# Optimization experiments

Hardware: AMD Instinct MI355X
Metric: run time of the kernel (lower is better)

Reference implementation:

```python
import jax, jax.numpy as jnp
import numpy as np

HIDDEN = 1024
NUM_EXPERTS = 8
TOP_K = 2
BATCH, SEQ = 4, 4096


def setup_inputs() -> dict:
    key = jax.random.key(0)
    ks = jax.random.split(key, 7)
    s = 0.02
    x = jax.random.normal(ks[0], (BATCH, SEQ, HIDDEN), dtype=jnp.float32)
    router_w = jax.random.normal(ks[1], (HIDDEN, NUM_EXPERTS), dtype=jnp.float32) * s
    router_b = jnp.zeros((NUM_EXPERTS,), dtype=jnp.float32)
    w1 = jax.random.normal(ks[2], (NUM_EXPERTS, HIDDEN, 2 * HIDDEN), dtype=jnp.float32) * s
    b1 = jnp.zeros((NUM_EXPERTS, 2 * HIDDEN), dtype=jnp.float32)
    w2 = jax.random.normal(ks[3], (NUM_EXPERTS, 2 * HIDDEN, HIDDEN), dtype=jnp.float32) * s
    b2 = jnp.zeros((NUM_EXPERTS, HIDDEN), dtype=jnp.float32)
    return {"x": x, "router_w": router_w, "router_b": router_b,
            "w1": w1, "b1": b1, "w2": w2, "b2": b2}


def reference(x, router_w, router_b, w1, b1, w2, b2):
    # Router: softmax over experts, then top-k and renormalize.
    logits = jnp.einsum("bsh,he->bse", x, router_w) + router_b        # [B,S,E]
    probs = jax.nn.softmax(logits, axis=-1)
    topk_p, topk_i = jax.lax.top_k(probs, TOP_K)                       # [B,S,K]
    topk_p = topk_p / jnp.sum(topk_p, axis=-1, keepdims=True)

    out = jnp.zeros_like(x)
    for e in range(NUM_EXPERTS):
        # combine weight for this expert (0 for tokens that didn't route here;
        # top_k indices are distinct so at most one slot matches)
        w = jnp.sum(jnp.where(topk_i == e, topk_p, 0.0), axis=-1)      # [B,S]
        h = jax.nn.relu(jnp.einsum("bsh,hf->bsf", x, w1[e]) + b1[e])   # [B,S,2H]
        y = jnp.einsum("bsf,fh->bsh", h, w2[e]) + b2[e]                # [B,S,H]
        out = out + w[..., None] * y
    return out
```

## Files before the change

### kernel.cpp

```cpp
#include <hip/hip_runtime.h>

#define HIDDEN 1024
#define FF 2048
#define NEXP 8
#define NTOK 16384
#define NPAIR (2 * NTOK)
#define MAXT 136

typedef short short8 __attribute__((ext_vector_type(8)));
typedef unsigned short ushort4v __attribute__((ext_vector_type(4)));
typedef float f32x4 __attribute__((ext_vector_type(4)));

__device__ __forceinline__ unsigned short f2b(float f) {
  union { float f; unsigned int u; } v; v.f = f;
  unsigned int u = v.u;
  return (unsigned short)((u + 0x7fffu + ((u >> 16) & 1u)) >> 16);
}
__device__ __forceinline__ float b2f(unsigned short b) {
  union { unsigned int u; float f; } v; v.u = ((unsigned int)b) << 16;
  return v.f;
}

__device__ __forceinline__ void gload16(const unsigned short* g, unsigned short* l) {
  __builtin_amdgcn_global_load_lds(
      (const __attribute__((address_space(1))) unsigned int*)g,
      (__attribute__((address_space(3))) unsigned int*)l,
      16, 0, 0);
}

#define PIPE_WAIT(n) do { \
    asm volatile("s_waitcnt vmcnt(" #n ")" ::: "memory"); \
    __builtin_amdgcn_sched_barrier(0); \
  } while (0)
#define ABAR do { \
    asm volatile("s_barrier" ::: "memory"); \
    __builtin_amdgcn_sched_barrier(0); \
  } while (0)

#define W2T_OFF 0ull
#define W1T_OFF (W2T_OFF + (unsigned long long)NEXP * HIDDEN * FF * 2)
#define XB_OFF  (W1T_OFF + (unsigned long long)NEXP * FF * HIDDEN * 2)
#define H_OFF   (XB_OFF + (unsigned long long)NTOK * HIDDEN * 2)
#define CNT_OFF (H_OFF + (unsigned long long)NPAIR * FF * 2)
#define PLIST_OFF (CNT_OFF + 256ull)
#define PW_OFF    (PLIST_OFF + (unsigned long long)NEXP * NTOK * 4)
#define TOPS_OFF  (PW_OFF + (unsigned long long)NPAIR * 4)
#define W0_OFF    (TOPS_OFF + (unsigned long long)NTOK * 4)
#define WQ_OFF    (W0_OFF + (unsigned long long)NTOK * 4)
#define YP_OFF    W1T_OFF
#define WS_NEED   (WQ_OFF + 4096ull)

__global__ void zero_out_k(float4* __restrict__ out) {
  out[(size_t)blockIdx.x * 256 + threadIdx.x] = float4{0.f, 0.f, 0.f, 0.f};
}

__global__ void transpose_cast_k(const float* __restrict__ in,
                                 unsigned short* __restrict__ out,
                                 int R, int C) {
  __shared__ float tile[32][33];
  const size_t eoff = (size_t)blockIdx.z * R * C;
  const float* inp = in + eoff;
  unsigned short* outp = out + eoff;
  const int c = threadIdx.x & 31;
  const int r0 = threadIdx.x >> 5;
  const int gr = blockIdx.y * 32, gc = blockIdx.x * 32;
#pragma unroll
  for (int i = 0; i < 4; i++) {
    int r = r0 + i * 8;
    tile[r][c] = inp[(size_t)(gr + r) * C + gc + c];
  }
  __syncthreads();
#pragma unroll
  for (int i = 0; i < 4; i++) {
    int r = r0 + i * 8;
    outp[(size_t)(gc + r) * R + gr + c] = f2b(tile[c][r]);
  }
}

__global__ void router_k(const float* __restrict__ x, const float* __restrict__ rw,
                         const float* __restrict__ rb, int* __restrict__ tops,
                         float* __restrict__ w0f, unsigned short* __restrict__ xb,
                         int* __restrict__ cnt) {
  if (blockIdx.x == 0 && threadIdx.x < NEXP) cnt[threadIdx.x] = 0;
  const int wid = threadIdx.x >> 6;
  const int lane = threadIdx.x & 63;
  const int t = blockIdx.x * 4 + wid;
  const float* xr = x + (size_t)t * HIDDEN;
  float acc[8];
#pragma unroll
  for (int e = 0; e < 8; e++) acc[e] = 0.f;
#pragma unroll
  for (int i = 0; i < 16; i++) {
    int hh = lane + 64 * i;
    float xv = xr[hh];
    const float4* rwp = reinterpret_cast<const float4*>(rw + (size_t)hh * 8);
    float4 a = rwp[0], b = rwp[1];
    acc[0] += xv * a.x; acc[1] += xv * a.y; acc[2] += xv * a.z; acc[3] += xv * a.w;
    acc[4] += xv * b.x; acc[5] += xv * b.y; acc[6] += xv * b.z; acc[7] += xv * b.w;
  }
  {
    const float4* xr4 = reinterpret_cast<const float4*>(xr);
    unsigned short* xbr = xb + (size_t)t * HIDDEN;
#pragma unroll
    for (int i = 0; i < 4; i++) {
      float4 f = xr4[lane + 64 * i];
      ushort4v o;
      o[0] = f2b(f.x); o[1] = f2b(f.y); o[2] = f2b(f.z); o[3] = f2b(f.w);
      *reinterpret_cast<ushort4v*>(&xbr[(lane + 64 * i) * 4]) = o;
    }
  }
#pragma unroll
  for (int off = 32; off; off >>= 1) {
#pragma unroll
    for (int e = 0; e < 8; e++) acc[e] += __shfl_xor(acc[e], off);
  }
  if (lane == 0) {
#pragma unroll
    for (int e = 0; e < 8; e++) acc[e] += rb[e];
    int i0 = 0; float m0 = acc[0];
#pragma unroll
    for (int e = 1; e < 8; e++) if (acc[e] > m0) { m0 = acc[e]; i0 = e; }
    int i1 = -1; float m1 = -1e30f;
#pragma unroll
    for (int e = 0; e < 8; e++) if (e != i0 && acc[e] > m1) { m1 = acc[e]; i1 = e; }
    float w0 = 1.f / (1.f + __expf(m1 - m0));
    tops[t] = i0 | (i1 << 4);
    w0f[t] = w0;
  }
}

__global__ __launch_bounds__(256)
void scatter_k(const int* __restrict__ tops, const float* __restrict__ w0f,
               int* __restrict__ cnt, int* __restrict__ plist, float* __restrict__ pw) {
  __shared__ int lcnt[NEXP];
  __shared__ int lbase[NEXP];
  const int tid = threadIdx.x;
  const int t = blockIdx.x * 256 + tid;
  if (tid < NEXP) lcnt[tid] = 0;
  __syncthreads();
  const int packed = tops[t];
  const int i0 = packed & 15, i1 = packed >> 4;
  const float w0 = w0f[t];
  const int s0 = atomicAdd(&lcnt[i0], 1);
  const int s1 = atomicAdd(&lcnt[i1], 1);
  __syncthreads();
  if (tid < NEXP) lbase[tid] = atomicAdd(&cnt[tid], lcnt[tid]);
  __syncthreads();
  plist[i0 * NTOK + lbase[i0] + s0] = 2 * t;
  plist[i1 * NTOK + lbase[i1] + s1] = 2 * t + 1;
  pw[2 * t] = w0;
  pw[2 * t + 1] = 1.f - w0;
}

__global__ void plan_k(const int* __restrict__ cnt, int* __restrict__ workq) {
  if (threadIdx.x == 0) {
    int idx = 0;
    for (int e = 0; e < NEXP; e++) {
      int nt = (cnt[e] + 255) >> 8;
      for (int m = 0; m < nt; m++) workq[idx++] = (e << 16) | m;
    }
    while (idx < MAXT) workq[idx++] = -1;
  }
}

__global__ __launch_bounds__(256)
void combine_k(const unsigned short* __restrict__ ypair, const float* __restrict__ pw,
               float* __restrict__ out) {
  const int t = blockIdx.x * 2 + (threadIdx.x >> 7);
  const int i = (threadIdx.x & 127) * 8;
  const float w0 = pw[2 * t], w1 = pw[2 * t + 1];
  const short8 y0 = *(const short8*)&ypair[(size_t)(2 * t) * HIDDEN + i];
  const short8 y1 = *(const short8*)&ypair[(size_t)(2 * t + 1) * HIDDEN + i];
  float* orow = out + (size_t)t * HIDDEN + i;
#pragma unroll
  for (int j = 0; j < 8; j++)
    orow[j] = w0 * b2f((unsigned short)y0[j]) + w1 * b2f((unsigned short)y1[j]);
}

template <int PHASE, int YP>
__global__ __launch_bounds__(512, 1)
void ffn_k(const unsigned short* __restrict__ xb, const unsigned short* __restrict__ wT,
           const float* __restrict__ bias, const unsigned short* __restrict__ hin,
           unsigned short* __restrict__ hout, float* __restrict__ out,
           const int* __restrict__ cnt, const int* __restrict__ plist,
           const float* __restrict__ pw, const int* __restrict__ workq) {
  constexpr int K = (PHASE == 1) ? HIDDEN : FF;
  constexpr int N = (PHASE == 1) ? FF : HIDDEN;
  constexpr int NT = K / 32;
  constexpr int NTN = N / 256;
  constexpr int NWG = MAXT * NTN;

  constexpr int q8 = NWG / 8;
  const int bid = blockIdx.x;
  const int wgid = (bid & 7) * q8 + (bid >> 3);
  const int mt = wgid / NTN;
  const int n0g = (wgid % NTN) * 256;

  const int w = workq[mt];
  if (w < 0) return;
  const int e = w >> 16;
  const int m0g = (w & 0xffff) * 256;
  const int mcnt = cnt[e];
  const int mrem = mcnt - m0g;

  __shared__ alignas(16) unsigned short S[3][512][32];
  __shared__ int rowpair[256];

  const int tid = threadIdx.x;
  if (tid < 256) rowpair[tid] = (tid < mrem) ? plist[e * NTOK + m0g + tid] : -1;
  __syncthreads();

  const int w8 = tid >> 6;
  const int lane = tid & 63;

  const int sslot = (lane & 3) ^ ((lane >> 2) & 3);
  const int rsub = lane >> 2;
  const unsigned short* wTe = wT + (size_t)e * N * K;

  const unsigned short* gS[4];
  int ldsRow[4];
#pragma unroll
  for (int j = 0; j < 4; j++) {
    const int gr = j * 128 + w8 * 16;
    ldsRow[j] = gr;
    const int r = gr + rsub;
    if (gr < 256) {
      int p = rowpair[r];
      if (p < 0) p = 0;
      const unsigned short* abase;
      if constexpr (PHASE == 1) abase = xb + (size_t)(p >> 1) * HIDDEN;
      else                      abase = hin + (size_t)p * FF;
      gS[j] = abase + sslot * 8;
    } else {
      gS[j] = wTe + (size_t)(n0g + (r - 256)) * K + sslot * 8;
    }
  }

  const int wr = (w8 >> 2) * 128;
  const int wc = (w8 & 3) * 64;
  const int fr = lane & 15;
  const int fg = lane >> 4;
  const int fsw = fr & 3;

  f32x4 acc[8][4];
#pragma unroll
  for (int i = 0; i < 8; i++)
#pragma unroll
    for (int j = 0; j < 4; j++) acc[i][j] = f32x4{0.f, 0.f, 0.f, 0.f};

#pragma unroll
  for (int b = 0; b < 3; b++)
#pragma unroll
    for (int j = 0; j < 4; j++)
      gload16(gS[j] + b * 32, &S[b][ldsRow[j]][0]);

  int cur = 0;
  for (int t = 0; t < NT; ++t) {
    if (t < NT - 2)       PIPE_WAIT(8);
    else if (t == NT - 2) PIPE_WAIT(4);
    else                  PIPE_WAIT(0);
    ABAR;

    short8 af[8], bf[4];
#pragma unroll
    for (int mi = 0; mi < 8; mi++)
      af[mi] = *(const short8*)&S[cur][wr + mi * 16 + fr][(fg ^ fsw) * 8];
#pragma unroll
    for (int ni = 0; ni < 4; ni++)
      bf[ni] = *(const short8*)&S[cur][256 + wc + ni * 16 + fr][(fg ^ fsw) * 8];
#pragma unroll
    for (int mi = 0; mi < 8; mi++)
#pragma unroll
      for (int ni = 0; ni < 4; ni++)
        acc[mi][ni] = __builtin_amdgcn_mfma_f32_16x16x32_bf16(af[mi], bf[ni], acc[mi][ni], 0, 0, 0);

    ABAR;

    if (t + 3 < NT) {
      const int kt = (t + 3) * 32;
#pragma unroll
      for (int j = 0; j < 4; j++)
        gload16(gS[j] + kt, &S[cur][ldsRow[j]][0]);
    }
    cur = (cur == 2) ? 0 : cur + 1;
  }

  float bv[4];
#pragma unroll
  for (int ni = 0; ni < 4; ni++) bv[ni] = bias[(size_t)e * N + n0g + wc + ni * 16 + fr];

#pragma unroll
  for (int mi = 0; mi < 8; mi++) {
#pragma unroll
    for (int r = 0; r < 4; r++) {
      int m = wr + mi * 16 + fg * 4 + r;
      if (m >= mrem) continue;
      int p = rowpair[m];
      if constexpr (PHASE == 1) {
        unsigned short* hr = hout + (size_t)p * FF + n0g;
#pragma unroll
        for (int ni = 0; ni < 4; ni++) {
          float v = acc[mi][ni][r] + bv[ni];
          hr[wc + ni * 16 + fr] = f2b(fmaxf(v, 0.f));
        }
      } else if constexpr (YP == 1) {
        unsigned short* yr = hout + (size_t)p * HIDDEN + n0g;
#pragma unroll
        for (int ni = 0; ni < 4; ni++) {
          float v = acc[mi][ni][r] + bv[ni];
          yr[wc + ni * 16 + fr] = f2b(v);
        }
      } else {
        float wgt = pw[p];
        float* orow = out + (size_t)(p >> 1) * HIDDEN + n0g;
#pragma unroll
        for (int ni = 0; ni < 4; ni++) {
          float v = (acc[mi][ni][r] + bv[ni]) * wgt;
          atomicAdd(&orow[wc + ni * 16 + fr], v);
        }
      }
    }
  }
}

extern "C" void kernel_launch(void* const* d_in, const int* in_sizes, int n_in,
                              void* d_out, int out_size, void* d_ws, size_t ws_size,
                              hipStream_t stream) {
  const float* x  = (const float*)d_in[0];
  const float* rw = (const float*)d_in[1];
  const float* rb = (const float*)d_in[2];
  const float* w1 = (const float*)d_in[3];
  const float* b1 = (const float*)d_in[4];
  const float* w2 = (const float*)d_in[5];
  const float* b2 = (const float*)d_in[6];
  float* out = (float*)d_out;
  char* ws = (char*)d_ws;

  unsigned short* w2t = (unsigned short*)(ws + W2T_OFF);
  unsigned short* w1t = (unsigned short*)(ws + W1T_OFF);
  unsigned short* xb  = (unsigned short*)(ws + XB_OFF);
  unsigned short* h   = (unsigned short*)(ws + H_OFF);
  int* cnt   = (int*)(ws + CNT_OFF);
  int* plist = (int*)(ws + PLIST_OFF);
  float* pwt = (float*)(ws + PW_OFF);
  int* tops  = (int*)(ws + TOPS_OFF);
  float* w0f = (float*)(ws + W0_OFF);
  int* workq = (int*)(ws + WQ_OFF);
  unsigned short* ypair = (unsigned short*)(ws + YP_OFF);

  const bool use_yp = (ws_size >= WS_NEED);

  if (!use_yp)
    hipLaunchKernelGGL(zero_out_k, dim3(16384), dim3(256), 0, stream, (float4*)out);
  hipLaunchKernelGGL(transpose_cast_k, dim3(FF / 32, HIDDEN / 32, NEXP), dim3(256), 0, stream,
                     w1, w1t, HIDDEN, FF);
  hipLaunchKernelGGL(transpose_cast_k, dim3(HIDDEN / 32, FF / 32, NEXP), dim3(256), 0, stream,
                     w2, w2t, FF, HIDDEN);
  hipLaunchKernelGGL(router_k, dim3(NTOK / 4), dim3(256), 0, stream, x, rw, rb, tops, w0f, xb, cnt);
  hipLaunchKernelGGL(scatter_k, dim3(NTOK / 256), dim3(256), 0, stream, tops, w0f, cnt, plist, pwt);
  hipLaunchKernelGGL(plan_k, dim3(1), dim3(64), 0, stream, cnt, workq);
  hipLaunchKernelGGL((ffn_k<1, 0>), dim3(MAXT * (FF / 256)), dim3(512), 0, stream,
                     xb, w1t, b1, (const unsigned short*)nullptr, h, (float*)nullptr,
                     cnt, plist, pwt, workq);
  if (use_yp) {
    hipLaunchKernelGGL((ffn_k<2, 1>), dim3(MAXT * (HIDDEN / 256)), dim3(512), 0, stream,
                       xb, w2t, b2, h, ypair, (float*)nullptr,
                       cnt, plist, pwt, workq);
    hipLaunchKernelGGL(combine_k, dim3(NTOK / 2), dim3(256), 0, stream, ypair, pwt, out);
  } else {
    hipLaunchKernelGGL((ffn_k<2, 0>), dim3(MAXT * (HIDDEN / 256)), dim3(512), 0, stream,
                       xb, w2t, b2, h, (unsigned short*)nullptr, out,
                       cnt, plist, pwt, workq);
  }
}
```

Baseline: 554.5 us.

## Restructure FFN GEMM main loop into 64-wide K tiles with interleaved four-stage pipeline

Replaces the triple-buffered 32-wide K loop with double-buffered 64-wide K tiles, with A and B split into separate half-tiles. Each iteration is divided into four MFMA sub-blocks, and global-to-LDS loads for the next tiles are interleaved between them, with s_setprio raised around the MFMA clusters. The goal is to overlap LDS reads, global loads and matrix math more finely and to cut barrier and waitcnt overhead per K step. The cost is many more barriers per iteration, a new XOR swizzle and a more fragile schedule in which a mistake could cause a race.

Measured after the change: 490.6 us. -11.5%, faster.

```diff
diff --git a/kernel.cpp b/kernel.cpp
--- a/kernel.cpp
+++ b/kernel.cpp
@@ -186,7 +186,8 @@
            const float* __restrict__ pw, const int* __restrict__ workq) {
   constexpr int K = (PHASE == 1) ? HIDDEN : FF;
   constexpr int N = (PHASE == 1) ? FF : HIDDEN;
-  constexpr int NT = K / 32;
+  constexpr int NKT = K / 64;
+  constexpr int NI = NKT / 2;
   constexpr int NTN = N / 256;
   constexpr int NWG = MAXT * NTN;
 
@@ -203,7 +204,8 @@
   const int mcnt = cnt[e];
   const int mrem = mcnt - m0g;
 
-  __shared__ alignas(16) unsigned short S[3][512][32];
+  __shared__ alignas(16) unsigned short As[2][2][128][64];
+  __shared__ alignas(16) unsigned short Bs[2][2][128][64];
   __shared__ int rowpair[256];
 
   const int tid = threadIdx.x;
@@ -212,35 +214,33 @@
 
   const int w8 = tid >> 6;
   const int lane = tid & 63;
-
-  const int sslot = (lane & 3) ^ ((lane >> 2) & 3);
-  const int rsub = lane >> 2;
+  const int lrow = lane >> 3;
+  const int gslot = (lane & 7) ^ lrow;
   const unsigned short* wTe = wT + (size_t)e * N * K;
 
-  const unsigned short* gS[4];
-  int ldsRow[4];
-#pragma unroll
-  for (int j = 0; j < 4; j++) {
-    const int gr = j * 128 + w8 * 16;
-    ldsRow[j] = gr;
-    const int r = gr + rsub;
-    if (gr < 256) {
+  const unsigned short* aP[2][2];
+  const unsigned short* bP[2][2];
+#pragma unroll
+  for (int h = 0; h < 2; h++) {
+#pragma unroll
+    for (int i = 0; i < 2; i++) {
+      const int r = h * 128 + w8 * 16 + i * 8 + lrow;
       int p = rowpair[r];
       if (p < 0) p = 0;
       const unsigned short* abase;
       if constexpr (PHASE == 1) abase = xb + (size_t)(p >> 1) * HIDDEN;
       else                      abase = hin + (size_t)p * FF;
-      gS[j] = abase + sslot * 8;
-    } else {
-      gS[j] = wTe + (size_t)(n0g + (r - 256)) * K + sslot * 8;
+      aP[h][i] = abase + gslot * 8;
+      bP[h][i] = wTe + (size_t)(n0g + r) * K + gslot * 8;
     }
   }
 
-  const int wr = (w8 >> 2) * 128;
-  const int wc = (w8 & 3) * 64;
+  const int hA = w8 >> 2;
+  const int hB = (w8 & 3) >> 1;
+  const int br0 = ((w8 & 3) & 1) * 64;
   const int fr = lane & 15;
   const int fg = lane >> 4;
-  const int fsw = fr & 3;
+  const int fr7 = fr & 7;
 
   f32x4 acc[8][4];
 #pragma unroll
@@ -248,43 +248,75 @@
 #pragma unroll
     for (int j = 0; j < 4; j++) acc[i][j] = f32x4{0.f, 0.f, 0.f, 0.f};
 
-#pragma unroll
-  for (int b = 0; b < 3; b++)
-#pragma unroll
-    for (int j = 0; j < 4; j++)
-      gload16(gS[j] + b * 32, &S[b][ldsRow[j]][0]);
-
-  int cur = 0;
-  for (int t = 0; t < NT; ++t) {
-    if (t < NT - 2)       PIPE_WAIT(8);
-    else if (t == NT - 2) PIPE_WAIT(4);
-    else                  PIPE_WAIT(0);
+  short8 af0[4][2], af1[4][2], bf[2][2];
+
+#define DSA(dst, d, mh) \
+  _Pragma("unroll") for (int mi2 = 0; mi2 < 4; mi2++) \
+  _Pragma("unroll") for (int kk = 0; kk < 2; kk++) \
+    dst[mi2][kk] = *(const short8*)&As[d][hA][(mh)*64 + mi2*16 + fr][((kk*4+fg) ^ fr7) * 8];
+#define DSB(d, nh) \
+  _Pragma("unroll") for (int ni2 = 0; ni2 < 2; ni2++) \
+  _Pragma("unroll") for (int kk = 0; kk < 2; kk++) \
+    bf[ni2][kk] = *(const short8*)&Bs[d][hB][br0 + (nh)*32 + ni2*16 + fr][((kk*4+fg) ^ fr7) * 8];
+#define MM(afx, mh, nh) \
+  __builtin_amdgcn_s_setprio(1); \
+  _Pragma("unroll") for (int mi2 = 0; mi2 < 4; mi2++) \
+  _Pragma("unroll") for (int ni2 = 0; ni2 < 2; ni2++) \
+  _Pragma("unroll") for (int kk = 0; kk < 2; kk++) \
+    acc[(mh)*4 + mi2][(nh)*2 + ni2] = __builtin_amdgcn_mfma_f32_16x16x32_bf16( \
+        afx[mi2][kk], bf[ni2][kk], acc[(mh)*4 + mi2][(nh)*2 + ni2], 0, 0, 0); \
+  __builtin_amdgcn_s_setprio(0);
+#define STA(d, h, tk) { gload16(aP[h][0] + (tk)*64, &As[d][h][w8*16][0]); \
+                        gload16(aP[h][1] + (tk)*64, &As[d][h][w8*16+8][0]); }
+#define STB(d, h, tk) { gload16(bP[h][0] + (tk)*64, &Bs[d][h][w8*16][0]); \
+                        gload16(bP[h][1] + (tk)*64, &Bs[d][h][w8*16+8][0]); }
+
+  STA(0, 0, 0) STA(0, 1, 0) STB(0, 0, 0) STB(0, 1, 0)
+  STA(1, 0, 1) STA(1, 1, 1)
+  PIPE_WAIT(4);
+  ABAR;
+
+  for (int i = 0; i < NI; ++i) {
+    const int t1 = 2 * i + 1, t2 = 2 * i + 2, t3 = 2 * i + 3;
+    const bool g = (i < NI - 1);
+
+    DSA(af0, 0, 0) DSB(0, 0)
+    STB(1, 0, t1)
+    ABAR; MM(af0, 0, 0) ABAR;
+    DSA(af1, 0, 1)
+    STB(1, 1, t1)
+    ABAR; MM(af1, 1, 0) ABAR;
+    DSB(0, 1)
+    if (g) STA(0, 0, t2)
+    ABAR; MM(af1, 1, 1) ABAR;
+    if (g) STA(0, 1, t2)
+    ABAR; MM(af0, 0, 1)
+    if (g) PIPE_WAIT(4); else PIPE_WAIT(0);
     ABAR;
 
-    short8 af[8], bf[4];
-#pragma unroll
-    for (int mi = 0; mi < 8; mi++)
-      af[mi] = *(const short8*)&S[cur][wr + mi * 16 + fr][(fg ^ fsw) * 8];
-#pragma unroll
-    for (int ni = 0; ni < 4; ni++)
-      bf[ni] = *(const short8*)&S[cur][256 + wc + ni * 16 + fr][(fg ^ fsw) * 8];
-#pragma unroll
-    for (int mi = 0; mi < 8; mi++)
-#pragma unroll
-      for (int ni = 0; ni < 4; ni++)
-        acc[mi][ni] = __builtin_amdgcn_mfma_f32_16x16x32_bf16(af[mi], bf[ni], acc[mi][ni], 0, 0, 0);
-
+    DSA(af0, 1, 0) DSB(1, 0)
+    if (g) STB(0, 0, t2)
+    ABAR; MM(af0, 0, 0) ABAR;
+    DSA(af1, 1, 1)
+    if (g) STB(0, 1, t2)
+    ABAR; MM(af1, 1, 0) ABAR;
+    DSB(1, 1)
+    if (g) STA(1, 0, t3)
+    ABAR; MM(af1, 1, 1) ABAR;
+    if (g) STA(1, 1, t3)
+    ABAR; MM(af0, 0, 1)
+    if (g) PIPE_WAIT(4); else PIPE_WAIT(0);
     ABAR;
-
-    if (t + 3 < NT) {
-      const int kt = (t + 3) * 32;
-#pragma unroll
-      for (int j = 0; j < 4; j++)
-        gload16(gS[j] + kt, &S[cur][ldsRow[j]][0]);
-    }
-    cur = (cur == 2) ? 0 : cur + 1;
-  }
-
+  }
+
+#undef DSA
+#undef DSB
+#undef MM
+#undef STA
+#undef STB
+
+  const int wr = hA * 128;
+  const int wc = (w8 & 3) * 64;
   float bv[4];
 #pragma unroll
   for (int ni = 0; ni < 4; ni++) bv[ni] = bias[(size_t)e * N + n0g + wc + ni * 16 + fr];
```
